# Optimization experiments

Hardware: AMD Instinct MI355X
Metric: run time of the kernel (lower is better)

Reference implementation:

```python
import jax, jax.numpy as jnp
import numpy as np

K = 3  # kernel size along all four dims (kernel_size=3, padding=2=K-1, circular)


def setup_inputs() -> dict:
    key = jax.random.key(0)
    k1, k2, k3 = jax.random.split(key, 3)
    b, c_in, c_out, s = 4, 64, 64, 16
    x = jax.random.normal(k1, (b, c_in, s, s, s, s), dtype=jnp.float32)
    # torch grouped Conv3d weight (out_c*K, c_in, K, K, K) viewed as (K, out_c, c_in, K, K, K):
    # group g (= kernel slice along dim 0) uses weight[g].
    weight = jax.random.normal(k2, (K, c_out, c_in, K, K, K), dtype=jnp.float32) * 0.05
    bias = jax.random.normal(k3, (c_out,), dtype=jnp.float32)
    return {"x": x, "weight": weight, "bias": bias}


def _conv4d_circular(x, weight, bias):
    k = weight.shape[0]
    p = k - 1
    lo, hi = (p + 1) // 2, p // 2  # circular pad split used by do_padding
    b, c = x.shape[0], x.shape[1]
    s0, s1, s2, s3 = x.shape[2:]
    c_out = weight.shape[1]
    # circular-pad the three inner spatial dims only (dim s0 handled via rolls)
    xp = jnp.pad(x, ((0, 0), (0, 0), (0, 0), (lo, hi), (lo, hi), (lo, hi)), mode='wrap')
    # fold s0 into batch: (b*s0, c, S1, S2, S3)
    xr = xp.transpose(0, 2, 1, 3, 4, 5).reshape(b * s0, c, s1 + p, s2 + p, s3 + p)
    # grouped conv with input replicated across groups == k independent VALID 3D convs
    conv = lambda w: jax.lax.conv_general_dilated(
        xr, w, window_strides=(1, 1, 1), padding='VALID',
        dimension_numbers=('NCDHW', 'OIDHW', 'NCDHW'))
    out = jax.vmap(conv)(weight)  # (k, b*s0, c_out, s1, s2, s3)
    out = out.reshape(k, b, s0, c_out, s1, s2, s3).transpose(0, 1, 3, 2, 4, 5, 6)
    # combine kernel slices along dim-0 axis: result[..., t] = sum_i out[i, ..., (t+i) % s0]
    rolled = jnp.stack([jnp.roll(out[i], -i, axis=2) for i in range(k)], axis=0)
    res = rolled.sum(axis=0) + bias[None, :, None, None, None, None]
    shift = (p + 1) // 2  # math.ceil(padding[0] / 2)
    res = jnp.roll(res, shift, axis=2)
    return res  # (b, c_out, s0, s1, s2, s3)


def reference(x, weight, bias):
    return _conv4d_circular(x, weight, bias)
```

## Files before the change

kernel.cpp:

```cpp
#include <hip/hip_runtime.h>

typedef unsigned short u16;
typedef __attribute__((ext_vector_type(8))) __bf16 bf16x8;
typedef __attribute__((ext_vector_type(8))) short short8;
typedef __attribute__((ext_vector_type(4))) float floatx4;

__device__ __forceinline__ u16 f2bf(float f){
  unsigned int x = __float_as_uint(f);
  unsigned int r = (x + 0x7fffu + ((x >> 16) & 1u)) >> 16;
  return (u16)r;
}

#define GLL(g, l) __builtin_amdgcn_global_load_lds( \
    (const __attribute__((address_space(1))) void*)(g), \
    (__attribute__((address_space(3))) void*)(l), 16, 0, 0)

__global__ void prep_kernel(const float* __restrict__ x, const float* __restrict__ w,
                            u16* __restrict__ xp, u16* __restrict__ wp){
  const int bx = blockIdx.x;
  const int tid = threadIdx.x;
  if (bx < 1024){
    const int y = bx & 15, t = (bx >> 4) & 15, b = bx >> 8;
    const float* src = x + (size_t)b*64*65536 + t*4096 + y*256 + tid;
    u16* dst = xp + (size_t)bx*16384 + tid*64;
#pragma unroll
    for (int oct = 0; oct < 8; ++oct){
      float v[8];
#pragma unroll
      for (int j = 0; j < 8; ++j)
        v[j] = src[(oct*8 + j)*65536];
      short8 vv;
#pragma unroll
      for (int j = 0; j < 8; ++j) vv[j] = (short)f2bf(v[j]);
      *(short8*)(dst + ((oct ^ (tid & 7))*8)) = vv;
    }
  } else {
    int idx = (bx - 1024)*256 + tid;
    if (idx < 81*64*64){
      int r  = idx;
      int dw = r % 3; r /= 3;
      int dz = r % 3; r /= 3;
      int dy = r % 3; r /= 3;
      int ci = r & 63; r >>= 6;
      int co = r & 63; r >>= 6;
      int dt = r;
      int tap = ((dt*3 + dy)*3 + dz)*3 + dw;
      int kc = ci >> 5, ci32 = ci & 31;
      wp[tap*4096 + kc*2048 + co*32 + ci32] = f2bf(w[idx]);
    }
  }
}

__global__ __launch_bounds__(256, 2) void conv4d_mfma_fast(
    const u16* __restrict__ xp, const u16* __restrict__ wp,
    const float* __restrict__ bias, float* __restrict__ out)
{
  __shared__ __attribute__((aligned(16))) u16 x_lds[16384];
  __shared__ __attribute__((aligned(16))) u16 a_lds[12288];

  const int bx = blockIdx.x;
  const int y = bx & 15, t = (bx >> 4) & 15, b = bx >> 8;
  const int tid  = threadIdx.x;
  const int lane = tid & 63;
  const int wv   = tid >> 6;
  const int wl   = lane & 15;
  const int q    = lane >> 4;

  floatx4 acc[4][4];
#pragma unroll
  for (int zi = 0; zi < 4; ++zi)
#pragma unroll
    for (int mi = 0; mi < 4; ++mi)
      acc[zi][mi] = (floatx4)0.0f;

  for (int dt = 0; dt < 3; ++dt){
    const int tt = (t + dt + 15) & 15;
    for (int dy = 0; dy < 3; ++dy){
      const int yy = (y + dy + 15) & 15;
      __syncthreads();
      {
        const u16* plane = xp + (size_t)(((b*16 + tt)*16) + yy) * 16384;
#pragma unroll
        for (int i = 0; i < 8; ++i)
          GLL(plane + wv*4096 + i*512 + lane*8, x_lds + wv*4096 + i*512);
      }
      for (int dz = 0; dz < 3; ++dz){
        const int tap0 = ((dt*3 + dy)*3 + dz)*3;
        __syncthreads();
        {
          const u16* asrc = wp + (size_t)tap0 * 4096;
#pragma unroll
          for (int i = 0; i < 6; ++i)
            GLL(asrc + wv*3072 + i*512 + lane*8, a_lds + wv*3072 + i*512);
        }
        __syncthreads();
#pragma unroll
        for (int dw = 0; dw < 3; ++dw){
          const int ww = (wl + dw + 15) & 15;
          const int wx = ww & 7;
#pragma unroll
          for (int kc = 0; kc < 2; ++kc){
            bf16x8 af[4];
#pragma unroll
            for (int mi = 0; mi < 4; ++mi)
              af[mi] = *(const bf16x8*)(a_lds + ((dw*2 + kc)*64 + mi*16 + wl)*32 + q*8);
            const int chunk = ((kc*4 + q) ^ wx)*8;
#pragma unroll
            for (int zi = 0; zi < 4; ++zi){
              const int zz = (wv*4 + zi + dz + 15) & 15;
              bf16x8 bf = *(const bf16x8*)(x_lds + (zz*16 + ww)*64 + chunk);
#pragma unroll
              for (int mi = 0; mi < 4; ++mi)
                acc[zi][mi] = __builtin_amdgcn_mfma_f32_16x16x32_bf16(af[mi], bf, acc[zi][mi], 0, 0, 0);
            }
          }
        }
      }
    }
  }

  float bvals[4][4];
#pragma unroll
  for (int mi = 0; mi < 4; ++mi)
#pragma unroll
    for (int r = 0; r < 4; ++r)
      bvals[mi][r] = bias[mi*16 + q*4 + r];

  float* ob = out + (size_t)b*64*65536 + t*4096 + y*256 + wl;
#pragma unroll
  for (int zi = 0; zi < 4; ++zi){
    const int z = wv*4 + zi;
#pragma unroll
    for (int mi = 0; mi < 4; ++mi){
#pragma unroll
      for (int r = 0; r < 4; ++r){
        const int co = mi*16 + q*4 + r;
        ob[(size_t)co*65536 + z*16] = acc[zi][mi][r] + bvals[mi][r];
      }
    }
  }
}

__global__ void repack_w_kernel(const float* __restrict__ w, u16* __restrict__ wp){
  int idx = blockIdx.x * 256 + threadIdx.x;
  if (idx >= 81*64*64) return;
  int cw  = idx & 31;
  int t1  = idx >> 5;
  int co  = t1 & 63; t1 >>= 6;
  int kc  = t1 & 1;  t1 >>= 1;
  int tap = t1;
  int dw = tap % 3, dz = (tap/3) % 3, dy = (tap/9) % 3, dt = tap/27;
  int ci = kc*32 + cw;
  int in_idx = ((((dt*64 + co)*64 + ci)*3 + dy)*3 + dz)*3 + dw;
  wp[idx] = f2bf(w[in_idx]);
}

__global__ __launch_bounds__(256, 2) void conv4d_mfma_kernel(
    const float* __restrict__ x, const u16* __restrict__ wp,
    const float* __restrict__ bias, float* __restrict__ out)
{
  __shared__ __attribute__((aligned(16))) u16 x_lds[256*72];
  __shared__ __attribute__((aligned(16))) u16 a_lds[3*2*64*32];
  const int bx = blockIdx.x;
  const int y = bx & 15, t = (bx >> 4) & 15, b = bx >> 8;
  const int tid  = threadIdx.x;
  const int lane = tid & 63;
  const int wv   = tid >> 6;
  const int wl   = lane & 15;
  const int q    = lane >> 4;
  floatx4 acc[4][4];
#pragma unroll
  for (int zi = 0; zi < 4; ++zi)
#pragma unroll
    for (int mi = 0; mi < 4; ++mi)
      acc[zi][mi] = (floatx4)0.0f;
  const float* xb = x + (size_t)b * 64 * 65536;
  for (int dt = 0; dt < 3; ++dt){
    const int tt = (t + dt + 15) & 15;
    for (int dy = 0; dy < 3; ++dy){
      const int yy = (y + dy + 15) & 15;
      __syncthreads();
      {
        const float* src = xb + tt*4096 + yy*256 + tid;
#pragma unroll
        for (int oct = 0; oct < 8; ++oct){
          float v[8];
#pragma unroll
          for (int j = 0; j < 8; ++j)
            v[j] = src[(size_t)(oct*8 + j) * 65536];
          short8 vv;
#pragma unroll
          for (int j = 0; j < 8; ++j) vv[j] = (short)f2bf(v[j]);
          *(short8*)(x_lds + tid*72 + oct*8) = vv;
        }
      }
      for (int dz = 0; dz < 3; ++dz){
        const int tap0 = ((dt*3 + dy)*3 + dz)*3;
        __syncthreads();
        {
          const u16* asrc = wp + (size_t)tap0 * 4096;
#pragma unroll
          for (int i = 0; i < 6; ++i){
            int e = (i*256 + tid) * 8;
            *(short8*)(a_lds + e) = *(const short8*)(asrc + e);
          }
        }
        __syncthreads();
#pragma unroll
        for (int dw = 0; dw < 3; ++dw){
          const int ww = (wl + dw + 15) & 15;
#pragma unroll
          for (int kc = 0; kc < 2; ++kc){
            bf16x8 af[4];
#pragma unroll
            for (int mi = 0; mi < 4; ++mi)
              af[mi] = *(const bf16x8*)(a_lds + ((dw*2 + kc)*64 + mi*16 + wl)*32 + q*8);
#pragma unroll
            for (int zi = 0; zi < 4; ++zi){
              const int zz = (wv*4 + zi + dz + 15) & 15;
              bf16x8 bf = *(const bf16x8*)(x_lds + (zz*16 + ww)*72 + kc*32 + q*8);
#pragma unroll
              for (int mi = 0; mi < 4; ++mi)
                acc[zi][mi] = __builtin_amdgcn_mfma_f32_16x16x32_bf16(af[mi], bf, acc[zi][mi], 0, 0, 0);
            }
          }
        }
      }
    }
  }
  float bvals[4][4];
#pragma unroll
  for (int mi = 0; mi < 4; ++mi)
#pragma unroll
    for (int r = 0; r < 4; ++r)
      bvals[mi][r] = bias[mi*16 + q*4 + r];
  float* ob = out + (size_t)b * 64 * 65536 + t*4096 + y*256 + wl;
#pragma unroll
  for (int zi = 0; zi < 4; ++zi){
    const int z = wv*4 + zi;
#pragma unroll
    for (int mi = 0; mi < 4; ++mi){
#pragma unroll
      for (int r = 0; r < 4; ++r){
        const int co = mi*16 + q*4 + r;
        ob[(size_t)co*65536 + z*16] = acc[zi][mi][r] + bvals[mi][r];
      }
    }
  }
}

extern "C" void kernel_launch(void* const* d_in, const int* in_sizes, int n_in,
                              void* d_out, int out_size, void* d_ws, size_t ws_size,
                              hipStream_t stream) {
  const float* x    = (const float*)d_in[0];
  const float* w    = (const float*)d_in[1];
  const float* bias = (const float*)d_in[2];
  float* out = (float*)d_out;

  const size_t xp_bytes = (size_t)1024 * 16384 * 2;
  const size_t wp_bytes = 81*64*64*2;
  if (ws_size >= xp_bytes + wp_bytes){
    u16* xp = (u16*)d_ws;
    u16* wp = (u16*)((char*)d_ws + xp_bytes);
    prep_kernel<<<1024 + 1296, 256, 0, stream>>>(x, w, xp, wp);
    conv4d_mfma_fast<<<1024, 256, 0, stream>>>(xp, wp, bias, out);
  } else {
    u16* wp = (u16*)d_ws;
    repack_w_kernel<<<1296, 256, 0, stream>>>(w, wp);
    conv4d_mfma_kernel<<<1024, 256, 0, stream>>>(x, wp, bias, out);
  }
}
```

Before: 261.9 us.

## Load weights directly from global into registers with software prefetch, drop weight LDS

Removes the LDS staging buffer for weights and the two barriers per dz step; each lane now reads its weight fragments straight from global/L2 and prefetches the next tap's fragments while issuing MFMAs on the current ones. Freeing the 24KB weight LDS allows the launch bound to rise to 3 blocks per CU. The cost is more global/L2 traffic, since every wave re-reads the weights instead of sharing them through LDS, plus extra registers for the double-buffered fragments, which may cause spilling under the tighter bound.

```diff
diff --git a/kernel.cpp b/kernel.cpp
--- a/kernel.cpp
+++ b/kernel.cpp
@@ -51,12 +51,11 @@
   }
 }
 
-__global__ __launch_bounds__(256, 2) void conv4d_mfma_fast(
+__global__ __launch_bounds__(256, 3) void conv4d_mfma_v3(
     const u16* __restrict__ xp, const u16* __restrict__ wp,
     const float* __restrict__ bias, float* __restrict__ out)
 {
   __shared__ __attribute__((aligned(16))) u16 x_lds[16384];
-  __shared__ __attribute__((aligned(16))) u16 a_lds[12288];
 
   const int bx = blockIdx.x;
   const int y = bx & 15, t = (bx >> 4) & 15, b = bx >> 8;
@@ -73,49 +72,51 @@
     for (int mi = 0; mi < 4; ++mi)
       acc[zi][mi] = (floatx4)0.0f;
 
-  for (int dt = 0; dt < 3; ++dt){
+  const u16* wbase = wp + wl*32 + q*8;
+
+  auto ldA = [&](int G, bf16x8* af){
+    const int dtdy = G / 18, g = G % 18;
+    const int dt = dtdy / 3, dy = dtdy % 3;
+    const int dz = g / 6, dw = (g % 6) >> 1, kc = g & 1;
+    const int tap = ((dt*3 + dy)*3 + dz)*3 + dw;
+    const u16* p = wbase + (tap*2 + kc)*2048;
+#pragma unroll
+    for (int mi = 0; mi < 4; ++mi)
+      af[mi] = *(const bf16x8*)(p + mi*512);
+  };
+
+  bf16x8 afc[4], afn[4];
+  ldA(0, afc);
+
+  for (int dtdy = 0; dtdy < 9; ++dtdy){
+    const int dt = dtdy / 3, dy = dtdy % 3;
     const int tt = (t + dt + 15) & 15;
-    for (int dy = 0; dy < 3; ++dy){
-      const int yy = (y + dy + 15) & 15;
-      __syncthreads();
-      {
-        const u16* plane = xp + (size_t)(((b*16 + tt)*16) + yy) * 16384;
-#pragma unroll
-        for (int i = 0; i < 8; ++i)
-          GLL(plane + wv*4096 + i*512 + lane*8, x_lds + wv*4096 + i*512);
-      }
-      for (int dz = 0; dz < 3; ++dz){
-        const int tap0 = ((dt*3 + dy)*3 + dz)*3;
-        __syncthreads();
-        {
-          const u16* asrc = wp + (size_t)tap0 * 4096;
-#pragma unroll
-          for (int i = 0; i < 6; ++i)
-            GLL(asrc + wv*3072 + i*512 + lane*8, a_lds + wv*3072 + i*512);
-        }
-        __syncthreads();
-#pragma unroll
-        for (int dw = 0; dw < 3; ++dw){
-          const int ww = (wl + dw + 15) & 15;
-          const int wx = ww & 7;
-#pragma unroll
-          for (int kc = 0; kc < 2; ++kc){
-            bf16x8 af[4];
-#pragma unroll
-            for (int mi = 0; mi < 4; ++mi)
-              af[mi] = *(const bf16x8*)(a_lds + ((dw*2 + kc)*64 + mi*16 + wl)*32 + q*8);
-            const int chunk = ((kc*4 + q) ^ wx)*8;
-#pragma unroll
-            for (int zi = 0; zi < 4; ++zi){
-              const int zz = (wv*4 + zi + dz + 15) & 15;
-              bf16x8 bf = *(const bf16x8*)(x_lds + (zz*16 + ww)*64 + chunk);
-#pragma unroll
-              for (int mi = 0; mi < 4; ++mi)
-                acc[zi][mi] = __builtin_amdgcn_mfma_f32_16x16x32_bf16(af[mi], bf, acc[zi][mi], 0, 0, 0);
-            }
-          }
-        }
-      }
+    const int yy = (y + dy + 15) & 15;
+    __syncthreads();
+    {
+      const u16* plane = xp + (size_t)(((b*16 + tt)*16) + yy) * 16384;
+#pragma unroll
+      for (int i = 0; i < 8; ++i)
+        GLL(plane + wv*4096 + i*512 + lane*8, x_lds + wv*4096 + i*512);
+    }
+    __syncthreads();
+#pragma unroll
+    for (int g = 0; g < 18; ++g){
+      const int dz = g / 6, dw = (g % 6) >> 1, kc = g & 1;
+      const int G = dtdy*18 + g;
+      ldA(G + 1 < 162 ? G + 1 : 161, afn);
+      const int ww = (wl + dw + 15) & 15;
+      const int chunk = ((kc*4 + q) ^ (ww & 7))*8;
+#pragma unroll
+      for (int zi = 0; zi < 4; ++zi){
+        const int zz = (wv*4 + zi + dz + 15) & 15;
+        bf16x8 bf = *(const bf16x8*)(x_lds + (zz*16 + ww)*64 + chunk);
+#pragma unroll
+        for (int mi = 0; mi < 4; ++mi)
+          acc[zi][mi] = __builtin_amdgcn_mfma_f32_16x16x32_bf16(afc[mi], bf, acc[zi][mi], 0, 0, 0);
+      }
+#pragma unroll
+      for (int mi = 0; mi < 4; ++mi) afc[mi] = afn[mi];
     }
   }
 
@@ -263,7 +264,7 @@
     u16* xp = (u16*)d_ws;
     u16* wp = (u16*)((char*)d_ws + xp_bytes);
     prep_kernel<<<1024 + 1296, 256, 0, stream>>>(x, w, xp, wp);
-    conv4d_mfma_fast<<<1024, 256, 0, stream>>>(xp, wp, bias, out);
+    conv4d_mfma_v3<<<1024, 256, 0, stream>>>(xp, wp, bias, out);
   } else {
     u16* wp = (u16*)d_ws;
     repack_w_kernel<<<1296, 256, 0, stream>>>(w, wp);
```

Result: slower. 396.6 us (+51.4%).

## Double-buffer weight tiles in LDS and remap block indices for locality

Applied to the files above, without the earlier changes.

Flattens the dt/dy/dz tap loops into a single 27-step loop and double-buffers the weight tile in LDS, prefetching the next tap's weights with async global-to-LDS loads while the MFMAs of the current tap run. This cuts the number of barriers per step. The x plane is still reloaded only at dz boundaries, where the pipeline drains. It also remaps blockIdx so that neighbouring blocks share batch and y-halves, aiming at better L2 reuse of the prepacked x planes. The cost is an extra 24KB of LDS per block, which may reduce occupancy below the target of 2 blocks per SIMD group.

```diff
diff --git a/kernel.cpp b/kernel.cpp
--- a/kernel.cpp
+++ b/kernel.cpp
@@ -51,15 +51,17 @@
   }
 }
 
-__global__ __launch_bounds__(256, 2) void conv4d_mfma_fast(
+__global__ __launch_bounds__(256, 2) void conv4d_mfma_v4(
     const u16* __restrict__ xp, const u16* __restrict__ wp,
     const float* __restrict__ bias, float* __restrict__ out)
 {
   __shared__ __attribute__((aligned(16))) u16 x_lds[16384];
-  __shared__ __attribute__((aligned(16))) u16 a_lds[12288];
+  __shared__ __attribute__((aligned(16))) u16 a_lds[2][12288];
 
   const int bx = blockIdx.x;
-  const int y = bx & 15, t = (bx >> 4) & 15, b = bx >> 8;
+  const int c = bx & 7, j = bx >> 3;
+  const int b = c >> 1, t = j >> 3, y = (c & 1)*8 + (j & 7);
+
   const int tid  = threadIdx.x;
   const int lane = tid & 63;
   const int wv   = tid >> 6;
@@ -73,49 +75,66 @@
     for (int mi = 0; mi < 4; ++mi)
       acc[zi][mi] = (floatx4)0.0f;
 
-  for (int dt = 0; dt < 3; ++dt){
+  auto stage_x = [&](int dtdy){
+    const int dt = dtdy / 3, dy = dtdy % 3;
     const int tt = (t + dt + 15) & 15;
-    for (int dy = 0; dy < 3; ++dy){
-      const int yy = (y + dy + 15) & 15;
-      __syncthreads();
-      {
-        const u16* plane = xp + (size_t)(((b*16 + tt)*16) + yy) * 16384;
-#pragma unroll
-        for (int i = 0; i < 8; ++i)
-          GLL(plane + wv*4096 + i*512 + lane*8, x_lds + wv*4096 + i*512);
-      }
-      for (int dz = 0; dz < 3; ++dz){
-        const int tap0 = ((dt*3 + dy)*3 + dz)*3;
-        __syncthreads();
-        {
-          const u16* asrc = wp + (size_t)tap0 * 4096;
-#pragma unroll
-          for (int i = 0; i < 6; ++i)
-            GLL(asrc + wv*3072 + i*512 + lane*8, a_lds + wv*3072 + i*512);
-        }
-        __syncthreads();
-#pragma unroll
-        for (int dw = 0; dw < 3; ++dw){
-          const int ww = (wl + dw + 15) & 15;
-          const int wx = ww & 7;
-#pragma unroll
-          for (int kc = 0; kc < 2; ++kc){
-            bf16x8 af[4];
-#pragma unroll
-            for (int mi = 0; mi < 4; ++mi)
-              af[mi] = *(const bf16x8*)(a_lds + ((dw*2 + kc)*64 + mi*16 + wl)*32 + q*8);
-            const int chunk = ((kc*4 + q) ^ wx)*8;
-#pragma unroll
-            for (int zi = 0; zi < 4; ++zi){
-              const int zz = (wv*4 + zi + dz + 15) & 15;
-              bf16x8 bf = *(const bf16x8*)(x_lds + (zz*16 + ww)*64 + chunk);
-#pragma unroll
-              for (int mi = 0; mi < 4; ++mi)
-                acc[zi][mi] = __builtin_amdgcn_mfma_f32_16x16x32_bf16(af[mi], bf, acc[zi][mi], 0, 0, 0);
-            }
-          }
-        }
-      }
+    const int yy = (y + dy + 15) & 15;
+    const u16* plane = xp + (size_t)(((b*16 + tt)*16) + yy) * 16384;
+#pragma unroll
+    for (int i = 0; i < 8; ++i)
+      GLL(plane + wv*4096 + i*512 + lane*8, x_lds + wv*4096 + i*512);
+  };
+  auto stage_a = [&](int s, int buf){
+    const int dtdy = s / 3, dz = s % 3;
+    const int tap0 = ((dtdy/3)*9 + (dtdy%3)*3 + dz)*3;
+    const u16* asrc = wp + (size_t)tap0 * 4096;
+#pragma unroll
+    for (int i = 0; i < 6; ++i)
+      GLL(asrc + wv*3072 + i*512 + lane*8, a_lds[buf] + wv*3072 + i*512);
+  };
+
+  stage_x(0);
+  stage_a(0, 0);
+  __syncthreads();
+
+  for (int s = 0; s < 27; ++s){
+    const int dz  = s % 3;
+    const int cur = s & 1;
+    const bool boundary = (dz == 2);
+    if (s + 1 < 27 && !boundary)
+      stage_a(s + 1, cur ^ 1);
+
+    const u16* ab = a_lds[cur];
+#pragma unroll
+    for (int dw = 0; dw < 3; ++dw){
+      const int ww = (wl + dw + 15) & 15;
+      const int wx = ww & 7;
+#pragma unroll
+      for (int kc = 0; kc < 2; ++kc){
+        bf16x8 af[4];
+#pragma unroll
+        for (int mi = 0; mi < 4; ++mi)
+          af[mi] = *(const bf16x8*)(ab + ((dw*2 + kc)*64 + mi*16 + wl)*32 + q*8);
+        const int chunk = ((kc*4 + q) ^ wx)*8;
+#pragma unroll
+        for (int zi = 0; zi < 4; ++zi){
+          const int zz = (wv*4 + zi + dz + 15) & 15;
+          bf16x8 bf = *(const bf16x8*)(x_lds + (zz*16 + ww)*64 + chunk);
+#pragma unroll
+          for (int mi = 0; mi < 4; ++mi)
+            acc[zi][mi] = __builtin_amdgcn_mfma_f32_16x16x32_bf16(af[mi], bf, acc[zi][mi], 0, 0, 0);
+        }
+      }
+    }
+
+    if (s + 1 >= 27) break;
+    if (boundary){
+      __syncthreads();
+      stage_x(s/3 + 1);
+      stage_a(s + 1, cur ^ 1);
+      __syncthreads();
+    } else {
+      __syncthreads();
     }
   }
 
@@ -263,7 +282,7 @@
     u16* xp = (u16*)d_ws;
     u16* wp = (u16*)((char*)d_ws + xp_bytes);
     prep_kernel<<<1024 + 1296, 256, 0, stream>>>(x, w, xp, wp);
-    conv4d_mfma_fast<<<1024, 256, 0, stream>>>(xp, wp, bias, out);
+    conv4d_mfma_v4<<<1024, 256, 0, stream>>>(xp, wp, bias, out);
   } else {
     u16* wp = (u16*)d_ws;
     repack_w_kernel<<<1296, 256, 0, stream>>>(w, wp);
```

New measurement: 256.4 us. 2.1% less time.
